# Kernel optimization log

Measured on AMD Instinct MI355X. Metric: run time of the kernel, lower is better.

## Reference

```python
import jax, jax.numpy as jnp
import numpy as np

TEMPERATURE = 0.07
NEG_INF = -9e15
EPS = 1e-12

def setup_inputs() -> dict:
    key = jax.random.key(0)
    k1, k2 = jax.random.split(key)
    N, D = 8192, 128
    features = jax.random.normal(k1, (N, D), dtype=jnp.float32)
    labels = jax.random.randint(k2, (N,), 0, 16, dtype=jnp.int64)
    return {"features": features, "labels": labels}

def reference(features, labels):
    N = features.shape[0]
    # L2 normalize rows (torch F.normalize: x / max(||x||, eps))
    norm = jnp.linalg.norm(features, axis=1, keepdims=True)
    f = features / jnp.maximum(norm, EPS)
    # [N, N] similarity
    sim = jnp.matmul(f, f.T) / TEMPERATURE
    eye = jnp.eye(N, dtype=bool)
    sim = jnp.where(eye, NEG_INF, sim)
    # positive-pair mask: same label, excluding self
    pos_mask = ((labels[:, None] == labels[None, :]) & ~eye).astype(sim.dtype)
    denom = jnp.exp(sim).sum(axis=1, keepdims=True)  # [N, 1]
    log_prob = sim - jnp.log(denom + EPS)
    loss = -(pos_mask * log_prob).sum(axis=1) / (pos_mask.sum(axis=1) + EPS)
    return loss.mean()
```

## Files before the change

kernel.cpp:

```cpp
#include <hip/hip_runtime.h>
#include <hip/hip_bf16.h>

#define TEMP_INV (1.0f / 0.07f)
#define EPS 1e-12f
#define C_EXP 20.609929155556625f
#define NUM_CLASSES 16
#define CS_BLOCKS 128

#define BM 256
#define BN 128
#define KD 128
#define NCHUNK 8
#define NPART 16

typedef __attribute__((ext_vector_type(4))) float f32x4;
typedef __attribute__((ext_vector_type(8))) short bf16x8;

__device__ __forceinline__ float bf2f(ushort u) {
    unsigned int x = ((unsigned int)u) << 16;
    return __uint_as_float(x);
}

__device__ __forceinline__ const bf16x8* lds_frag(const ushort* base, int r, int slot) {
    int sw = slot ^ (r & 7);
    return reinterpret_cast<const bf16x8*>(
        reinterpret_cast<const char*>(base) + r * 256 + sw * 16);
}

__global__ void normalize_kernel(const float* __restrict__ feat,
                                 ushort* __restrict__ fb,
                                 float* __restrict__ sq,
                                 int N, int D) {
    int wave = (blockIdx.x * blockDim.x + threadIdx.x) >> 6;
    int lane = threadIdx.x & 63;
    if (wave >= N) return;
    const float* row = feat + (size_t)wave * D;
    float s = 0.f;
    for (int k = lane; k < D; k += 64) { float v = row[k]; s += v * v; }
    #pragma unroll
    for (int off = 1; off < 64; off <<= 1) s += __shfl_xor(s, off);
    float scale = 1.0f / fmaxf(sqrtf(s), EPS);
    ushort* orow = fb + (size_t)wave * D;
    float q = 0.f;
    for (int k = lane; k < D; k += 64) {
        __hip_bfloat16 h = __float2bfloat16(row[k] * scale);
        ushort u = *reinterpret_cast<ushort*>(&h);
        orow[k] = u;
        float hv = bf2f(u);
        q += hv * hv;
    }
    #pragma unroll
    for (int off = 1; off < 64; off <<= 1) q += __shfl_xor(q, off);
    if (lane == 0) sq[wave] = q;
}

__global__ __launch_bounds__(256) void classsum_kernel(
    const ushort* __restrict__ fb,
    const int* __restrict__ labels,
    float* __restrict__ g,
    float* __restrict__ cntf,
    int N, int D) {
    __shared__ float lds[2][NUM_CLASSES][128];
    __shared__ float ldc[2][NUM_CLASSES];
    const int d    = threadIdx.x & 127;
    const int half = threadIdx.x >> 7;
    #pragma unroll
    for (int c = 0; c < NUM_CLASSES; c++) lds[half][c][d] = 0.f;
    if (d < NUM_CLASSES) ldc[half][d] = 0.f;
    __syncthreads();

    const int rows_per_block = N / CS_BLOCKS;
    const int half_rows = rows_per_block >> 1;
    const int r0 = blockIdx.x * rows_per_block + half * half_rows;
    for (int r = r0; r < r0 + half_rows; r++) {
        int lab = labels[r];
        lds[half][lab][d] += bf2f(fb[(size_t)r * D + d]);
        if (d == 0) ldc[half][lab] += 1.f;
    }
    __syncthreads();

    for (int c = half; c < NUM_CLASSES; c += 2)
        atomicAdd(&g[c * D + d], lds[0][c][d] + lds[1][c][d]);
    if (threadIdx.x < NUM_CLASSES)
        atomicAdd(&cntf[threadIdx.x], ldc[0][threadIdx.x] + ldc[1][threadIdx.x]);
}

__global__ __launch_bounds__(512, 2) void supcon_denom(
    const ushort* __restrict__ fb,
    float* __restrict__ denom_part,
    int N, int D) {

    __shared__ __align__(16) ushort As[BM * KD];
    __shared__ __align__(16) ushort Bs[2][BN * KD];

    const int tid  = threadIdx.x;
    const int lane = tid & 63;
    const int w    = tid >> 6;
    const int wr   = w >> 1;
    const int wc   = w & 1;
    const int r16  = lane & 15;
    const int g4   = lane >> 4;

    const int rowbase = blockIdx.y * BM;
    const int col0    = blockIdx.x * (BN * NCHUNK);

    {
        const ushort* gA = fb + (size_t)rowbase * KD;
        #pragma unroll
        for (int i = 0; i < 8; i++) {
            int c = i * 512 + tid;
            bf16x8 v = *reinterpret_cast<const bf16x8*>(gA + c * 8);
            int dst = c ^ ((c >> 4) & 7);
            *reinterpret_cast<bf16x8*>(&As[dst * 8]) = v;
        }
        const ushort* gB = fb + (size_t)col0 * KD;
        #pragma unroll
        for (int i = 0; i < 4; i++) {
            int c = i * 512 + tid;
            bf16x8 v = *reinterpret_cast<const bf16x8*>(gB + c * 8);
            int dst = c ^ ((c >> 4) & 7);
            *reinterpret_cast<bf16x8*>(&Bs[0][dst * 8]) = v;
        }
    }
    __syncthreads();

    float pd[4][4];
    #pragma unroll
    for (int m = 0; m < 4; m++)
        #pragma unroll
        for (int i = 0; i < 4; i++) pd[m][i] = 0.f;

    int cur = 0;
    for (int c = 0; c < NCHUNK; c++) {
        bf16x8 pre0, pre1, pre2, pre3;
        if (c + 1 < NCHUNK) {
            const ushort* gB = fb + (size_t)(col0 + (c + 1) * BN) * KD;
            pre0 = *reinterpret_cast<const bf16x8*>(gB + (0 * 512 + tid) * 8);
            pre1 = *reinterpret_cast<const bf16x8*>(gB + (1 * 512 + tid) * 8);
            pre2 = *reinterpret_cast<const bf16x8*>(gB + (2 * 512 + tid) * 8);
            pre3 = *reinterpret_cast<const bf16x8*>(gB + (3 * 512 + tid) * 8);
        }

        f32x4 acc[4][4];
        #pragma unroll
        for (int m = 0; m < 4; m++)
            #pragma unroll
            for (int n = 0; n < 4; n++) acc[m][n] = f32x4{0.f, 0.f, 0.f, 0.f};

        const ushort* bbase = Bs[cur];
        #pragma unroll
        for (int ks = 0; ks < 4; ks++) {
            const int slot = ks * 4 + g4;
            bf16x8 av[4], bv[4];
            #pragma unroll
            for (int m = 0; m < 4; m++)
                av[m] = *lds_frag(As, wr * 64 + m * 16 + r16, slot);
            #pragma unroll
            for (int n = 0; n < 4; n++)
                bv[n] = *lds_frag(bbase, wc * 64 + n * 16 + r16, slot);
            #pragma unroll
            for (int m = 0; m < 4; m++)
                #pragma unroll
                for (int n = 0; n < 4; n++)
                    acc[m][n] = __builtin_amdgcn_mfma_f32_16x16x32_bf16(av[m], bv[n], acc[m][n], 0, 0, 0);
        }

        #pragma unroll
        for (int m = 0; m < 4; m++)
            #pragma unroll
            for (int n = 0; n < 4; n++)
                #pragma unroll
                for (int i = 0; i < 4; i++)
                    pd[m][i] += __builtin_amdgcn_exp2f(acc[m][n][i] * C_EXP);

        if (c + 1 < NCHUNK) {
            ushort* dstb = Bs[cur ^ 1];
            int ch;
            ch = 0 * 512 + tid; *reinterpret_cast<bf16x8*>(&dstb[(ch ^ ((ch >> 4) & 7)) * 8]) = pre0;
            ch = 1 * 512 + tid; *reinterpret_cast<bf16x8*>(&dstb[(ch ^ ((ch >> 4) & 7)) * 8]) = pre1;
            ch = 2 * 512 + tid; *reinterpret_cast<bf16x8*>(&dstb[(ch ^ ((ch >> 4) & 7)) * 8]) = pre2;
            ch = 3 * 512 + tid; *reinterpret_cast<bf16x8*>(&dstb[(ch ^ ((ch >> 4) & 7)) * 8]) = pre3;
        }
        __syncthreads();
        cur ^= 1;
    }

    #pragma unroll
    for (int off = 1; off < 16; off <<= 1)
        #pragma unroll
        for (int m = 0; m < 4; m++)
            #pragma unroll
            for (int i = 0; i < 4; i++)
                pd[m][i] += __shfl_xor(pd[m][i], off);

    if (r16 == 0) {
        const int part = blockIdx.x * 2 + wc;
        #pragma unroll
        for (int m = 0; m < 4; m++)
            #pragma unroll
            for (int i = 0; i < 4; i++) {
                int r = rowbase + wr * 64 + m * 16 + g4 * 4 + i;
                denom_part[(size_t)r * NPART + part] = pd[m][i];
            }
    }
}

__global__ void rowloss_kernel(const ushort* __restrict__ fb,
                               const int* __restrict__ labels,
                               const float* __restrict__ denom_part,
                               const float* __restrict__ sq,
                               const float* __restrict__ g,
                               const float* __restrict__ cntf,
                               float* __restrict__ rowloss,
                               int N, int D) {
    int r    = (blockIdx.x * blockDim.x + threadIdx.x) >> 6;
    int lane = threadIdx.x & 63;
    if (r >= N) return;
    int lab = labels[r];
    const ushort* frow = fb + (size_t)r * D;
    const float*  grow = g + lab * D;
    float p = 0.f;
    for (int k = lane; k < D; k += 64) p += bf2f(frow[k]) * grow[k];
    #pragma unroll
    for (int off = 1; off < 64; off <<= 1) p += __shfl_xor(p, off);

    float dsum = (lane < NPART) ? denom_part[(size_t)r * NPART + lane] : 0.f;
    #pragma unroll
    for (int off = 1; off < NPART; off <<= 1) dsum += __shfl_xor(dsum, off);

    if (lane == 0) {
        float sqr    = sq[r];
        float possum = (p - sqr) * TEMP_INV;
        float cnt    = cntf[lab] - 1.0f;
        float dn     = dsum - __builtin_amdgcn_exp2f(sqr * C_EXP);
        rowloss[r]   = -(possum - cnt * logf(dn + EPS)) / (cnt + EPS);
    }
}

__global__ void reduce_kernel(const float* __restrict__ rowloss,
                              float* __restrict__ out, int N) {
    __shared__ float sdata[16];
    float s = 0.f;
    for (int r = threadIdx.x; r < N; r += blockDim.x) s += rowloss[r];
    #pragma unroll
    for (int off = 1; off < 64; off <<= 1) s += __shfl_xor(s, off);
    int wv = threadIdx.x >> 6;
    if ((threadIdx.x & 63) == 0) sdata[wv] = s;
    __syncthreads();
    if (threadIdx.x == 0) {
        float t = 0.f;
        int nw = (int)(blockDim.x >> 6);
        for (int i = 0; i < nw; i++) t += sdata[i];
        out[0] = t / (float)N;
    }
}

extern "C" void kernel_launch(void* const* d_in, const int* in_sizes, int n_in,
                              void* d_out, int out_size, void* d_ws, size_t ws_size,
                              hipStream_t stream) {
    const float* feat = (const float*)d_in[0];
    const int* labels = (const int*)d_in[1];
    const int N = in_sizes[1];
    const int D = in_sizes[0] / N;

    char* ws = (char*)d_ws;
    ushort* fb = (ushort*)ws;
    size_t off = (size_t)N * D * sizeof(ushort);
    float* g     = (float*)(ws + off);  off += (size_t)NUM_CLASSES * D * sizeof(float);
    float* cntf  = (float*)(ws + off);  off += (size_t)NUM_CLASSES * sizeof(float);
    size_t zbytes = (size_t)(NUM_CLASSES * D + NUM_CLASSES) * sizeof(float);
    float* sq         = (float*)(ws + off); off += (size_t)N * sizeof(float);
    float* rowloss    = (float*)(ws + off); off += (size_t)N * sizeof(float);
    float* denom_part = (float*)(ws + off);

    hipMemsetAsync(g, 0, zbytes, stream);

    normalize_kernel<<<(N + 3) / 4, 256, 0, stream>>>(feat, fb, sq, N, D);
    classsum_kernel<<<CS_BLOCKS, 256, 0, stream>>>(fb, labels, g, cntf, N, D);

    dim3 grid(N / (BN * NCHUNK), N / BM);
    supcon_denom<<<grid, 512, 0, stream>>>(fb, denom_part, N, D);

    rowloss_kernel<<<(N + 3) / 4, 256, 0, stream>>>(fb, labels, denom_part, sq, g, cntf, rowloss, N, D);
    reduce_kernel<<<1, 1024, 0, stream>>>(rowloss, (float*)d_out, N);
}
```

Baseline: 57.54 us.

## Fuse all stages into one cooperative persistent kernel with grid syncs

Replaces the memset and five separate kernel launches with a single cooperative kernel of 256 blocks. Grid-wide syncs separate the normalize/class-sum, class-sum reduction, similarity-denominator GEMM, row loss and final reduction phases. Class sums now go through per-block partial buffers instead of atomics. The aim is to remove launch gaps and intermediate kernel boundaries. In exchange it adds grid barrier costs, and the GEMM phase runs with one 512-thread block per CU using 128KB of LDS.

Result: slower. 172.1 us (+199.1%).

```diff
diff --git a/kernel.cpp b/kernel.cpp
--- a/kernel.cpp
+++ b/kernel.cpp
@@ -1,11 +1,13 @@
 #include <hip/hip_runtime.h>
 #include <hip/hip_bf16.h>
+#include <hip/hip_cooperative_groups.h>
+
+namespace cg = cooperative_groups;
 
 #define TEMP_INV (1.0f / 0.07f)
 #define EPS 1e-12f
 #define C_EXP 20.609929155556625f
 #define NUM_CLASSES 16
-#define CS_BLOCKS 128
 
 #define BM 256
 #define BN 128
@@ -27,231 +29,267 @@
         reinterpret_cast<const char*>(base) + r * 256 + sw * 16);
 }
 
-__global__ void normalize_kernel(const float* __restrict__ feat,
-                                 ushort* __restrict__ fb,
-                                 float* __restrict__ sq,
-                                 int N, int D) {
-    int wave = (blockIdx.x * blockDim.x + threadIdx.x) >> 6;
-    int lane = threadIdx.x & 63;
-    if (wave >= N) return;
-    const float* row = feat + (size_t)wave * D;
-    float s = 0.f;
-    for (int k = lane; k < D; k += 64) { float v = row[k]; s += v * v; }
-    #pragma unroll
-    for (int off = 1; off < 64; off <<= 1) s += __shfl_xor(s, off);
-    float scale = 1.0f / fmaxf(sqrtf(s), EPS);
-    ushort* orow = fb + (size_t)wave * D;
-    float q = 0.f;
-    for (int k = lane; k < D; k += 64) {
-        __hip_bfloat16 h = __float2bfloat16(row[k] * scale);
-        ushort u = *reinterpret_cast<ushort*>(&h);
-        orow[k] = u;
-        float hv = bf2f(u);
-        q += hv * hv;
-    }
-    #pragma unroll
-    for (int off = 1; off < 64; off <<= 1) q += __shfl_xor(q, off);
-    if (lane == 0) sq[wave] = q;
-}
-
-__global__ __launch_bounds__(256) void classsum_kernel(
-    const ushort* __restrict__ fb,
+__global__ __launch_bounds__(512) void supcon_all(
+    const float* __restrict__ feat,
     const int* __restrict__ labels,
+    ushort* __restrict__ fb,
+    float* __restrict__ sq,
+    float* __restrict__ g_part,
+    float* __restrict__ cnt_part,
     float* __restrict__ g,
     float* __restrict__ cntf,
-    int N, int D) {
-    __shared__ float lds[2][NUM_CLASSES][128];
-    __shared__ float ldc[2][NUM_CLASSES];
-    const int d    = threadIdx.x & 127;
-    const int half = threadIdx.x >> 7;
-    #pragma unroll
-    for (int c = 0; c < NUM_CLASSES; c++) lds[half][c][d] = 0.f;
-    if (d < NUM_CLASSES) ldc[half][d] = 0.f;
-    __syncthreads();
-
-    const int rows_per_block = N / CS_BLOCKS;
-    const int half_rows = rows_per_block >> 1;
-    const int r0 = blockIdx.x * rows_per_block + half * half_rows;
-    for (int r = r0; r < r0 + half_rows; r++) {
-        int lab = labels[r];
-        lds[half][lab][d] += bf2f(fb[(size_t)r * D + d]);
-        if (d == 0) ldc[half][lab] += 1.f;
-    }
-    __syncthreads();
-
-    for (int c = half; c < NUM_CLASSES; c += 2)
-        atomicAdd(&g[c * D + d], lds[0][c][d] + lds[1][c][d]);
-    if (threadIdx.x < NUM_CLASSES)
-        atomicAdd(&cntf[threadIdx.x], ldc[0][threadIdx.x] + ldc[1][threadIdx.x]);
-}
-
-__global__ __launch_bounds__(512, 2) void supcon_denom(
-    const ushort* __restrict__ fb,
     float* __restrict__ denom_part,
-    int N, int D) {
-
-    __shared__ __align__(16) ushort As[BM * KD];
-    __shared__ __align__(16) ushort Bs[2][BN * KD];
+    float* __restrict__ block_loss,
+    float* __restrict__ out,
+    int N) {
+
+    cg::grid_group gridg = cg::this_grid();
+    __shared__ __align__(16) char smem[131072];
 
     const int tid  = threadIdx.x;
     const int lane = tid & 63;
-    const int w    = tid >> 6;
-    const int wr   = w >> 1;
-    const int wc   = w & 1;
-    const int r16  = lane & 15;
-    const int g4   = lane >> 4;
-
-    const int rowbase = blockIdx.y * BM;
-    const int col0    = blockIdx.x * (BN * NCHUNK);
+    const int wv   = tid >> 6;
+    const int bx   = blockIdx.x;
 
     {
-        const ushort* gA = fb + (size_t)rowbase * KD;
+        float* lg = (float*)smem;
+        float* lc = (float*)(smem + 65536);
+        for (int i = lane; i < NUM_CLASSES * 128; i += 64) lg[wv * 2048 + i] = 0.f;
+        if (lane < NUM_CLASSES) lc[wv * 16 + lane] = 0.f;
+
+        const int r0 = bx * 32 + wv * 4;
+        for (int rr = 0; rr < 4; rr++) {
+            const int r = r0 + rr;
+            const float2 v = *reinterpret_cast<const float2*>(feat + (size_t)r * KD + lane * 2);
+            float s = v.x * v.x + v.y * v.y;
+            #pragma unroll
+            for (int off = 1; off < 64; off <<= 1) s += __shfl_xor(s, off);
+            const float scale = 1.0f / fmaxf(sqrtf(s), EPS);
+
+            __hip_bfloat16 h0 = __float2bfloat16(v.x * scale);
+            __hip_bfloat16 h1 = __float2bfloat16(v.y * scale);
+            ushort u0 = *reinterpret_cast<ushort*>(&h0);
+            ushort u1 = *reinterpret_cast<ushort*>(&h1);
+            float q0 = bf2f(u0), q1 = bf2f(u1);
+            float q = q0 * q0 + q1 * q1;
+            #pragma unroll
+            for (int off = 1; off < 64; off <<= 1) q += __shfl_xor(q, off);
+            if (lane == 0) sq[r] = q;
+
+            unsigned int pack = (unsigned int)u0 | ((unsigned int)u1 << 16);
+            *reinterpret_cast<unsigned int*>(fb + (size_t)r * KD + lane * 2) = pack;
+
+            const int lab = labels[r];
+            lg[wv * 2048 + lab * 128 + lane * 2]     += q0;
+            lg[wv * 2048 + lab * 128 + lane * 2 + 1] += q1;
+            if (lane == 0) lc[wv * 16 + lab] += 1.f;
+        }
+        __syncthreads();
+        for (int i = tid; i < NUM_CLASSES * 128; i += 512) {
+            float acc = 0.f;
+            #pragma unroll
+            for (int w8 = 0; w8 < 8; w8++) acc += lg[w8 * 2048 + i];
+            g_part[(size_t)bx * 2048 + i] = acc;
+        }
+        if (tid < NUM_CLASSES) {
+            float acc = 0.f;
+            #pragma unroll
+            for (int w8 = 0; w8 < 8; w8++) acc += lc[w8 * 16 + tid];
+            cnt_part[bx * NUM_CLASSES + tid] = acc;
+        }
+    }
+    gridg.sync();
+
+    if (bx < NUM_CLASSES) {
+        const int c = bx;
+        float* lr  = (float*)smem;
+        float* lr2 = (float*)(smem + 2048);
+        const int d = tid & 127, seg = tid >> 7;
+        float acc = 0.f;
+        for (int b = seg * 64; b < seg * 64 + 64; b++)
+            acc += g_part[(size_t)b * 2048 + c * 128 + d];
+        lr[seg * 128 + d] = acc;
+
+        float cv = 0.f;
+        if (tid < 256) cv = cnt_part[tid * NUM_CLASSES + c];
         #pragma unroll
-        for (int i = 0; i < 8; i++) {
-            int c = i * 512 + tid;
-            bf16x8 v = *reinterpret_cast<const bf16x8*>(gA + c * 8);
-            int dst = c ^ ((c >> 4) & 7);
-            *reinterpret_cast<bf16x8*>(&As[dst * 8]) = v;
-        }
-        const ushort* gB = fb + (size_t)col0 * KD;
-        #pragma unroll
-        for (int i = 0; i < 4; i++) {
-            int c = i * 512 + tid;
-            bf16x8 v = *reinterpret_cast<const bf16x8*>(gB + c * 8);
-            int dst = c ^ ((c >> 4) & 7);
-            *reinterpret_cast<bf16x8*>(&Bs[0][dst * 8]) = v;
-        }
-    }
-    __syncthreads();
-
-    float pd[4][4];
-    #pragma unroll
-    for (int m = 0; m < 4; m++)
-        #pragma unroll
-        for (int i = 0; i < 4; i++) pd[m][i] = 0.f;
-
-    int cur = 0;
-    for (int c = 0; c < NCHUNK; c++) {
-        bf16x8 pre0, pre1, pre2, pre3;
-        if (c + 1 < NCHUNK) {
-            const ushort* gB = fb + (size_t)(col0 + (c + 1) * BN) * KD;
-            pre0 = *reinterpret_cast<const bf16x8*>(gB + (0 * 512 + tid) * 8);
-            pre1 = *reinterpret_cast<const bf16x8*>(gB + (1 * 512 + tid) * 8);
-            pre2 = *reinterpret_cast<const bf16x8*>(gB + (2 * 512 + tid) * 8);
-            pre3 = *reinterpret_cast<const bf16x8*>(gB + (3 * 512 + tid) * 8);
-        }
-
-        f32x4 acc[4][4];
+        for (int off = 1; off < 64; off <<= 1) cv += __shfl_xor(cv, off);
+        if (tid < 256 && lane == 0) lr2[wv] = cv;
+        __syncthreads();
+        if (tid < 128) g[c * 128 + tid] = lr[tid] + lr[128 + tid] + lr[256 + tid] + lr[384 + tid];
+        if (tid == 0)  cntf[c] = lr2[0] + lr2[1] + lr2[2] + lr2[3];
+    }
+    gridg.sync();
+
+    {
+        ushort* As = (ushort*)smem;
+        ushort* Bs0 = (ushort*)(smem + 65536);
+        ushort* Bs1 = (ushort*)(smem + 65536 + 32768);
+
+        const int w    = wv;
+        const int wr   = w >> 1;
+        const int wc   = w & 1;
+        const int r16  = lane & 15;
+        const int g4   = lane >> 4;
+
+        const int rowblock = bx >> 3;
+        const int colgroup = bx & 7;
+        const int rowbase  = rowblock * BM;
+        const int col0     = colgroup * (BN * NCHUNK);
+
+        {
+            const ushort* gA = fb + (size_t)rowbase * KD;
+            #pragma unroll
+            for (int i = 0; i < 8; i++) {
+                int c = i * 512 + tid;
+                bf16x8 v = *reinterpret_cast<const bf16x8*>(gA + c * 8);
+                int dst = c ^ ((c >> 4) & 7);
+                *reinterpret_cast<bf16x8*>(&As[dst * 8]) = v;
+            }
+            const ushort* gB = fb + (size_t)col0 * KD;
+            #pragma unroll
+            for (int i = 0; i < 4; i++) {
+                int c = i * 512 + tid;
+                bf16x8 v = *reinterpret_cast<const bf16x8*>(gB + c * 8);
+                int dst = c ^ ((c >> 4) & 7);
+                *reinterpret_cast<bf16x8*>(&Bs0[dst * 8]) = v;
+            }
+        }
+        __syncthreads();
+
+        float pd[4][4];
         #pragma unroll
         for (int m = 0; m < 4; m++)
             #pragma unroll
-            for (int n = 0; n < 4; n++) acc[m][n] = f32x4{0.f, 0.f, 0.f, 0.f};
-
-        const ushort* bbase = Bs[cur];
+            for (int i = 0; i < 4; i++) pd[m][i] = 0.f;
+
+        int cur = 0;
+        for (int c = 0; c < NCHUNK; c++) {
+            bf16x8 pre0, pre1, pre2, pre3;
+            if (c + 1 < NCHUNK) {
+                const ushort* gB = fb + (size_t)(col0 + (c + 1) * BN) * KD;
+                pre0 = *reinterpret_cast<const bf16x8*>(gB + (0 * 512 + tid) * 8);
+                pre1 = *reinterpret_cast<const bf16x8*>(gB + (1 * 512 + tid) * 8);
+                pre2 = *reinterpret_cast<const bf16x8*>(gB + (2 * 512 + tid) * 8);
+                pre3 = *reinterpret_cast<const bf16x8*>(gB + (3 * 512 + tid) * 8);
+            }
+
+            f32x4 acc[4][4];
+            #pragma unroll
+            for (int m = 0; m < 4; m++)
+                #pragma unroll
+                for (int n = 0; n < 4; n++) acc[m][n] = f32x4{0.f, 0.f, 0.f, 0.f};
+
+            const ushort* bbase = cur ? Bs1 : Bs0;
+            #pragma unroll
+            for (int ks = 0; ks < 4; ks++) {
+                const int slot = ks * 4 + g4;
+                bf16x8 av[4], bv[4];
+                #pragma unroll
+                for (int m = 0; m < 4; m++)
+                    av[m] = *lds_frag(As, wr * 64 + m * 16 + r16, slot);
+                #pragma unroll
+                for (int n = 0; n < 4; n++)
+                    bv[n] = *lds_frag(bbase, wc * 64 + n * 16 + r16, slot);
+                #pragma unroll
+                for (int m = 0; m < 4; m++)
+                    #pragma unroll
+                    for (int n = 0; n < 4; n++)
+                        acc[m][n] = __builtin_amdgcn_mfma_f32_16x16x32_bf16(av[m], bv[n], acc[m][n], 0, 0, 0);
+            }
+
+            #pragma unroll
+            for (int m = 0; m < 4; m++)
+                #pragma unroll
+                for (int n = 0; n < 4; n++)
+                    #pragma unroll
+                    for (int i = 0; i < 4; i++)
+                        pd[m][i] += __builtin_amdgcn_exp2f(acc[m][n][i] * C_EXP);
+
+            if (c + 1 < NCHUNK) {
+                ushort* dstb = cur ? Bs0 : Bs1;
+                int ch;
+                ch = 0 * 512 + tid; *reinterpret_cast<bf16x8*>(&dstb[(ch ^ ((ch >> 4) & 7)) * 8]) = pre0;
+                ch = 1 * 512 + tid; *reinterpret_cast<bf16x8*>(&dstb[(ch ^ ((ch >> 4) & 7)) * 8]) = pre1;
+                ch = 2 * 512 + tid; *reinterpret_cast<bf16x8*>(&dstb[(ch ^ ((ch >> 4) & 7)) * 8]) = pre2;
+                ch = 3 * 512 + tid; *reinterpret_cast<bf16x8*>(&dstb[(ch ^ ((ch >> 4) & 7)) * 8]) = pre3;
+            }
+            __syncthreads();
+            cur ^= 1;
+        }
+
         #pragma unroll
-        for (int ks = 0; ks < 4; ks++) {
-            const int slot = ks * 4 + g4;
-            bf16x8 av[4], bv[4];
+        for (int off = 1; off < 16; off <<= 1)
             #pragma unroll
             for (int m = 0; m < 4; m++)
-                av[m] = *lds_frag(As, wr * 64 + m * 16 + r16, slot);
-            #pragma unroll
-            for (int n = 0; n < 4; n++)
-                bv[n] = *lds_frag(bbase, wc * 64 + n * 16 + r16, slot);
+                #pragma unroll
+                for (int i = 0; i < 4; i++)
+                    pd[m][i] += __shfl_xor(pd[m][i], off);
+
+        if (r16 == 0) {
+            const int part = colgroup * 2 + wc;
             #pragma unroll
             for (int m = 0; m < 4; m++)
                 #pragma unroll
-                for (int n = 0; n < 4; n++)
-                    acc[m][n] = __builtin_amdgcn_mfma_f32_16x16x32_bf16(av[m], bv[n], acc[m][n], 0, 0, 0);
-        }
-
+                for (int i = 0; i < 4; i++) {
+                    int r = rowbase + wr * 64 + m * 16 + g4 * 4 + i;
+                    denom_part[(size_t)r * NPART + part] = pd[m][i];
+                }
+        }
+    }
+    gridg.sync();
+
+    {
+        float* lsum = (float*)smem;
+        const int r0 = bx * 32 + wv * 4;
+        float wloss = 0.f;
+        for (int rr = 0; rr < 4; rr++) {
+            const int r = r0 + rr;
+            const int lab = labels[r];
+            unsigned int pk = *reinterpret_cast<const unsigned int*>(fb + (size_t)r * KD + lane * 2);
+            float f0 = bf2f((ushort)(pk & 0xffff));
+            float f1 = bf2f((ushort)(pk >> 16));
+            const float2 gv = *reinterpret_cast<const float2*>(g + lab * 128 + lane * 2);
+            float p = f0 * gv.x + f1 * gv.y;
+            #pragma unroll
+            for (int off = 1; off < 64; off <<= 1) p += __shfl_xor(p, off);
+
+            float dsum = (lane < NPART) ? denom_part[(size_t)r * NPART + lane] : 0.f;
+            #pragma unroll
+            for (int off = 1; off < NPART; off <<= 1) dsum += __shfl_xor(dsum, off);
+
+            if (lane == 0) {
+                float sqr    = sq[r];
+                float possum = (p - sqr) * TEMP_INV;
+                float cnt    = cntf[lab] - 1.0f;
+                float dn     = dsum - __builtin_amdgcn_exp2f(sqr * C_EXP);
+                wloss += -(possum - cnt * logf(dn + EPS)) / (cnt + EPS);
+            }
+        }
+        if (lane == 0) lsum[wv] = wloss;
+        __syncthreads();
+        if (tid == 0) {
+            float t = 0.f;
+            #pragma unroll
+            for (int i = 0; i < 8; i++) t += lsum[i];
+            block_loss[bx] = t;
+        }
+    }
+    gridg.sync();
+
+    if (bx == 0) {
+        float* lr = (float*)smem;
+        float s = (tid < 256) ? block_loss[tid] : 0.f;
         #pragma unroll
-        for (int m = 0; m < 4; m++)
-            #pragma unroll
-            for (int n = 0; n < 4; n++)
-                #pragma unroll
-                for (int i = 0; i < 4; i++)
-                    pd[m][i] += __builtin_amdgcn_exp2f(acc[m][n][i] * C_EXP);
-
-        if (c + 1 < NCHUNK) {
-            ushort* dstb = Bs[cur ^ 1];
-            int ch;
-            ch = 0 * 512 + tid; *reinterpret_cast<bf16x8*>(&dstb[(ch ^ ((ch >> 4) & 7)) * 8]) = pre0;
-            ch = 1 * 512 + tid; *reinterpret_cast<bf16x8*>(&dstb[(ch ^ ((ch >> 4) & 7)) * 8]) = pre1;
-            ch = 2 * 512 + tid; *reinterpret_cast<bf16x8*>(&dstb[(ch ^ ((ch >> 4) & 7)) * 8]) = pre2;
-            ch = 3 * 512 + tid; *reinterpret_cast<bf16x8*>(&dstb[(ch ^ ((ch >> 4) & 7)) * 8]) = pre3;
-        }
-        __syncthreads();
-        cur ^= 1;
-    }
-
-    #pragma unroll
-    for (int off = 1; off < 16; off <<= 1)
-        #pragma unroll
-        for (int m = 0; m < 4; m++)
-            #pragma unroll
-            for (int i = 0; i < 4; i++)
-                pd[m][i] += __shfl_xor(pd[m][i], off);
-
-    if (r16 == 0) {
-        const int part = blockIdx.x * 2 + wc;
-        #pragma unroll
-        for (int m = 0; m < 4; m++)
-            #pragma unroll
-            for (int i = 0; i < 4; i++) {
-                int r = rowbase + wr * 64 + m * 16 + g4 * 4 + i;
-                denom_part[(size_t)r * NPART + part] = pd[m][i];
-            }
-    }
-}
-
-__global__ void rowloss_kernel(const ushort* __restrict__ fb,
-                               const int* __restrict__ labels,
-                               const float* __restrict__ denom_part,
-                               const float* __restrict__ sq,
-                               const float* __restrict__ g,
-                               const float* __restrict__ cntf,
-                               float* __restrict__ rowloss,
-                               int N, int D) {
-    int r    = (blockIdx.x * blockDim.x + threadIdx.x) >> 6;
-    int lane = threadIdx.x & 63;
-    if (r >= N) return;
-    int lab = labels[r];
-    const ushort* frow = fb + (size_t)r * D;
-    const float*  grow = g + lab * D;
-    float p = 0.f;
-    for (int k = lane; k < D; k += 64) p += bf2f(frow[k]) * grow[k];
-    #pragma unroll
-    for (int off = 1; off < 64; off <<= 1) p += __shfl_xor(p, off);
-
-    float dsum = (lane < NPART) ? denom_part[(size_t)r * NPART + lane] : 0.f;
-    #pragma unroll
-    for (int off = 1; off < NPART; off <<= 1) dsum += __shfl_xor(dsum, off);
-
-    if (lane == 0) {
-        float sqr    = sq[r];
-        float possum = (p - sqr) * TEMP_INV;
-        float cnt    = cntf[lab] - 1.0f;
-        float dn     = dsum - __builtin_amdgcn_exp2f(sqr * C_EXP);
-        rowloss[r]   = -(possum - cnt * logf(dn + EPS)) / (cnt + EPS);
-    }
-}
-
-__global__ void reduce_kernel(const float* __restrict__ rowloss,
-                              float* __restrict__ out, int N) {
-    __shared__ float sdata[16];
-    float s = 0.f;
-    for (int r = threadIdx.x; r < N; r += blockDim.x) s += rowloss[r];
-    #pragma unroll
-    for (int off = 1; off < 64; off <<= 1) s += __shfl_xor(s, off);
-    int wv = threadIdx.x >> 6;
-    if ((threadIdx.x & 63) == 0) sdata[wv] = s;
-    __syncthreads();
-    if (threadIdx.x == 0) {
-        float t = 0.f;
-        int nw = (int)(blockDim.x >> 6);
-        for (int i = 0; i < nw; i++) t += sdata[i];
-        out[0] = t / (float)N;
+        for (int off = 1; off < 64; off <<= 1) s += __shfl_xor(s, off);
+        if (lane == 0) lr[wv] = s;
+        __syncthreads();
+        if (tid == 0) {
+            float t = 0.f;
+            #pragma unroll
+            for (int i = 0; i < 8; i++) t += lr[i];
+            out[0] = t / (float)N;
+        }
     }
 }
 
@@ -260,27 +298,27 @@
                               hipStream_t stream) {
     const float* feat = (const float*)d_in[0];
     const int* labels = (const int*)d_in[1];
-    const int N = in_sizes[1];
+    int N = in_sizes[1];
     const int D = in_sizes[0] / N;
+    (void)D;
 
     char* ws = (char*)d_ws;
-    ushort* fb = (ushort*)ws;
-    size_t off = (size_t)N * D * sizeof(ushort);
-    float* g     = (float*)(ws + off);  off += (size_t)NUM_CLASSES * D * sizeof(float);
-    float* cntf  = (float*)(ws + off);  off += (size_t)NUM_CLASSES * sizeof(float);
-    size_t zbytes = (size_t)(NUM_CLASSES * D + NUM_CLASSES) * sizeof(float);
-    float* sq         = (float*)(ws + off); off += (size_t)N * sizeof(float);
-    float* rowloss    = (float*)(ws + off); off += (size_t)N * sizeof(float);
-    float* denom_part = (float*)(ws + off);
-
-    hipMemsetAsync(g, 0, zbytes, stream);
-
-    normalize_kernel<<<(N + 3) / 4, 256, 0, stream>>>(feat, fb, sq, N, D);
-    classsum_kernel<<<CS_BLOCKS, 256, 0, stream>>>(fb, labels, g, cntf, N, D);
-
-    dim3 grid(N / (BN * NCHUNK), N / BM);
-    supcon_denom<<<grid, 512, 0, stream>>>(fb, denom_part, N, D);
-
-    rowloss_kernel<<<(N + 3) / 4, 256, 0, stream>>>(fb, labels, denom_part, sq, g, cntf, rowloss, N, D);
-    reduce_kernel<<<1, 1024, 0, stream>>>(rowloss, (float*)d_out, N);
+    size_t off = 0;
+    ushort* fb        = (ushort*)(ws + off); off += (size_t)N * KD * sizeof(ushort);
+    float* sq         = (float*)(ws + off);  off += (size_t)N * sizeof(float);
+    float* g_part     = (float*)(ws + off);  off += (size_t)256 * NUM_CLASSES * KD * sizeof(float);
+    float* cnt_part   = (float*)(ws + off);  off += (size_t)256 * NUM_CLASSES * sizeof(float);
+    float* g          = (float*)(ws + off);  off += (size_t)NUM_CLASSES * KD * sizeof(float);
+    float* cntf       = (float*)(ws + off);  off += (size_t)NUM_CLASSES * sizeof(float);
+    float* denom_part = (float*)(ws + off);  off += (size_t)N * NPART * sizeof(float);
+    float* block_loss = (float*)(ws + off);  off += (size_t)256 * sizeof(float);
+    float* outp       = (float*)d_out;
+
+    void* args[] = {
+        (void*)&feat, (void*)&labels, (void*)&fb, (void*)&sq,
+        (void*)&g_part, (void*)&cnt_part, (void*)&g, (void*)&cntf,
+        (void*)&denom_part, (void*)&block_loss, (void*)&outp, (void*)&N
+    };
+    hipLaunchCooperativeKernel((const void*)supcon_all,
+                               dim3(N / 32), dim3(512), args, 0, stream);
 }
```
